# Optimization experiments

Hardware: AMD Instinct MI355X
Metric: run time of the kernel (lower is better)

Reference implementation:

```python
import jax, jax.numpy as jnp
import numpy as np

_SAMPLING_EPS = 1e-5


def setup_inputs() -> dict:
    key = jax.random.key(0)
    ks = jax.random.split(key, 7)
    N, V, H = 256, 128000, 200  # num_seqs, vocab_size, output-history length
    logits = jax.random.normal(ks[0], (N, V), dtype=jnp.float32)
    output_tokens = jax.random.randint(ks[1], (N, H), 0, V, dtype=jnp.int32)
    presence_penalties = jax.random.uniform(ks[2], (N,), jnp.float32, 0.0, 2.0)
    frequency_penalties = jax.random.uniform(ks[3], (N,), jnp.float32, 0.0, 2.0)
    temperatures = jax.random.uniform(ks[4], (N,), jnp.float32, 0.5, 1.5)
    top_ps = jax.random.uniform(ks[5], (N,), jnp.float32, 0.5, 1.0)
    top_ks = jax.random.randint(ks[6], (N,), 1, 1000, dtype=jnp.int32)
    return {
        "logits": logits,
        "presence_penalties": presence_penalties,
        "frequency_penalties": frequency_penalties,
        "temperatures": temperatures,
        "top_ps": top_ps,
        "output_tokens": output_tokens,
        "top_ks": top_ks,
    }


def reference(logits, presence_penalties, frequency_penalties, temperatures,
              top_ps, output_tokens, top_ks):
    N, V = logits.shape

    # ---- _apply_penalties: bincount of previously generated tokens per row ----
    rows = jnp.arange(N)[:, None]  # [N,1] broadcast against [N,H] token ids
    bin_counts = jnp.zeros((N, V), logits.dtype).at[rows, output_tokens].add(1.0)
    # rows are skipped when both penalties are < eps (original builds an index list)
    active = ((presence_penalties >= _SAMPLING_EPS) |
              (frequency_penalties >= _SAMPLING_EPS))[:, None]
    presence_mask = (bin_counts > 0.0).astype(logits.dtype)
    penalty = (frequency_penalties[:, None] * bin_counts
               + presence_penalties[:, None] * presence_mask)
    logits = logits - jnp.where(active, penalty, jnp.zeros((), logits.dtype))

    # ---- temperature scaling + softmax ----
    logits = logits / temperatures[:, None]
    probs = jax.nn.softmax(logits, axis=-1)

    # ---- _apply_top_p_top_k: sort desc, cumsum, mask, unsort ----
    probs_idx = jnp.argsort(-probs, axis=-1)                    # descending order
    probs_sort = jnp.take_along_axis(probs, probs_idx, axis=-1)
    probs_sum = jnp.cumsum(probs_sort, axis=-1)
    top_p_mask = (probs_sum - probs_sort) > top_ps[:, None]     # exclusive cumsum > p
    probs_sort = jnp.where(top_p_mask, 0.0, probs_sort)
    top_k_mask = jnp.arange(V, dtype=top_ks.dtype)[None, :] >= top_ks[:, None]
    probs_sort = jnp.where(top_k_mask, 0.0, probs_sort)
    inv_idx = jnp.argsort(probs_idx, axis=-1)                   # unsort permutation
    filtered_probs = jnp.take_along_axis(probs_sort, inv_idx, axis=-1)
    return filtered_probs
```

## Files before the change

kernel.cpp:

```cpp
#include <hip/hip_runtime.h>
#include <stdint.h>

#define NB 4096
#define BSH 20
#define RSH 14
#define HS 512
#define HM 511
#define CAP 8192
#define PCAP 4096
#define NRB 2048
#define NT 1024

typedef unsigned long long ull;

__device__ __forceinline__ unsigned mono_u32(float x) {
    unsigned b = __float_as_uint(x);
    return (b & 0x80000000u) ? ~b : (b | 0x80000000u);
}
__device__ __forceinline__ float inv_mono(unsigned u) {
    unsigned b = (u & 0x80000000u) ? (u & 0x7fffffffu) : ~u;
    return __uint_as_float(b);
}

__device__ __forceinline__ float compute_x(float l, int cnt,
                                           float pres, float freq, float t) {
    float pen = __fadd_rn(__fmul_rn(freq, (float)cnt), (cnt > 0) ? pres : 0.0f);
    return __fdiv_rn(__fsub_rn(l, pen), t);
}

__device__ __forceinline__ int hash_lookup(const int* hkey, const int* hval, int v) {
    unsigned h = ((unsigned)v * 2654435761u) >> 23;
    while (true) {
        int kk = hkey[h];
        if (kk == v) return hval[h];
        if (kk == -1) return 0;
        h = (h + 1) & HM;
    }
}

__device__ int suffix_cut(unsigned* hc, int* sct, int* sct2, int k, int tid, int* sh) {
    if (tid == 0) *sh = -1;
    const int BPT = NB / NT;
    int base = tid * BPT;
    int acc = 0;
#pragma unroll
    for (int q = BPT - 1; q >= 0; --q) { acc += (int)hc[base + q]; hc[base + q] = (unsigned)acc; }
    sct[tid] = acc;
    __syncthreads();
    int* a = sct; int* b2 = sct2;
    for (int s = 1; s < NT; s <<= 1) {
        int v = a[tid] + ((tid + s < NT) ? a[tid + s] : 0);
        __syncthreads();
        b2[tid] = v;
        __syncthreads();
        int* tmp = a; a = b2; b2 = tmp;
    }
    int above = (tid < NT - 1) ? a[tid + 1] : 0;
    int best = -1;
#pragma unroll
    for (int q = BPT - 1; q >= 0; --q)
        if ((int)hc[base + q] + above >= k) { best = base + q; break; }
    if (best >= 0) atomicMax(sh, best);
    __syncthreads();
    int r = *sh;
    __syncthreads();
    return r;
}

__global__ __launch_bounds__(NT) void k_fused(
    const float* __restrict__ logits, const int* __restrict__ tokens,
    const float* __restrict__ pres_v, const float* __restrict__ freq_v,
    const float* __restrict__ temps, const float* __restrict__ topp_v,
    const int* __restrict__ topk_v, int V, int H, float* __restrict__ out)
{
    __shared__ ull skey[CAP];
    __shared__ ull hreg[4096];
    __shared__ int sct[NT], sct2[NT];
    __shared__ int hkey[HS], hval[HS];
    __shared__ float esum_s, corr_s;
    __shared__ int cut_s, lcnt_s, rb_s, pcnt_s;

    unsigned* hc = (unsigned*)hreg;
    unsigned* rh = (unsigned*)hreg;
    ull* tmpc = hreg;
    float* se = (float*)hreg;
    float* bs1 = (float*)sct;
    float* bs2 = (float*)sct2;

    int row = blockIdx.x, tid = threadIdx.x;
    for (int b = tid; b < NB; b += NT) hc[b] = 0u;
    for (int i = tid; i < HS; i += NT) { hkey[i] = -1; hval[i] = 0; }
    if (tid == 0) { esum_s = 0.f; corr_s = 0.f; lcnt_s = 0; rb_s = 0; pcnt_s = 0; }
    __syncthreads();

    const int* trow = tokens + (size_t)row * H;
    for (int i = tid; i < H; i += NT) {
        int v = trow[i];
        unsigned h = ((unsigned)v * 2654435761u) >> 23;
        while (true) {
            int prev = atomicCAS(&hkey[h], -1, v);
            if (prev == -1 || prev == v) { atomicAdd(&hval[h], 1); break; }
            h = (h + 1) & HM;
        }
    }

    float t = temps[row];
    float r = __fdiv_rn(1.0f, t);
    float pres = pres_v[row], freq = freq_v[row];
    int active = (pres >= 1e-5f) || (freq >= 1e-5f);
    int k = topk_v[row];
    const float* lrow = logits + (size_t)row * V;
    const float4* l4p = (const float4*)lrow;
    int V4 = V >> 2;
    __syncthreads();

    int S4 = V4 >> 4;
    for (int j = tid; j < S4; j += NT) {
        int c = j >> 6;
        int g = (((c << 4) + (c & 15)) << 6) | (j & 63);
        if (g < V4) {
            float4 A = l4p[g];
#pragma unroll
            for (int jj = 0; jj < 4; ++jj)
                atomicAdd(&hc[mono_u32(__fmul_rn((&A.x)[jj], r)) >> BSH], 1u);
        }
    }
    __syncthreads();
    float ms = (S4 > 0) ? ((float)k * (float)(S4 << 2) / (float)V) : 0.0f;
    int req = (int)(ms + 8.0f * sqrtf(ms) + 16.0f);
    int bT = (S4 > 0) ? suffix_cut(hc, sct, sct2, req, tid, &cut_s) : 0;
    int thr = bT - 1; if (thr < 0) thr = 0;
    for (int b = tid; b < NB; b += NT) hc[b] = 0u;
    __syncthreads();

    float4* o4p = (float4*)(out + (size_t)row * V);
    const float4 z4 = make_float4(0.f, 0.f, 0.f, 0.f);
    float es0 = 0.f, es1 = 0.f, es2 = 0.f, es3 = 0.f;
    int i = tid;
    for (; i + 7 * NT < V4; i += 8 * NT) {
        float4 arr[8];
#pragma unroll
        for (int q = 0; q < 8; ++q) arr[q] = l4p[i + q * NT];
#pragma unroll
        for (int q = 0; q < 8; ++q) o4p[i + q * NT] = z4;
#pragma unroll
        for (int q = 0; q < 8; ++q) {
            int vb = (i + q * NT) << 2;
            float x0 = __fmul_rn(arr[q].x, r), x1 = __fmul_rn(arr[q].y, r);
            float x2 = __fmul_rn(arr[q].z, r), x3 = __fmul_rn(arr[q].w, r);
            es0 += __expf(x0); es1 += __expf(x1); es2 += __expf(x2); es3 += __expf(x3);
            unsigned u0 = mono_u32(x0), u1 = mono_u32(x1);
            unsigned u2 = mono_u32(x2), u3 = mono_u32(x3);
            if ((int)(u0 >> BSH) >= thr) {
                atomicAdd(&hc[u0 >> BSH], 1u);
                int pos = atomicAdd(&lcnt_s, 1);
                if (pos < CAP) skey[pos] = ((ull)u0 << 32) | (unsigned)~(unsigned)(vb);
            }
            if ((int)(u1 >> BSH) >= thr) {
                atomicAdd(&hc[u1 >> BSH], 1u);
                int pos = atomicAdd(&lcnt_s, 1);
                if (pos < CAP) skey[pos] = ((ull)u1 << 32) | (unsigned)~(unsigned)(vb + 1);
            }
            if ((int)(u2 >> BSH) >= thr) {
                atomicAdd(&hc[u2 >> BSH], 1u);
                int pos = atomicAdd(&lcnt_s, 1);
                if (pos < CAP) skey[pos] = ((ull)u2 << 32) | (unsigned)~(unsigned)(vb + 2);
            }
            if ((int)(u3 >> BSH) >= thr) {
                atomicAdd(&hc[u3 >> BSH], 1u);
                int pos = atomicAdd(&lcnt_s, 1);
                if (pos < CAP) skey[pos] = ((ull)u3 << 32) | (unsigned)~(unsigned)(vb + 3);
            }
        }
    }
    for (; i < V4; i += NT) {
        float4 A = l4p[i];
        o4p[i] = z4;
#pragma unroll
        for (int j = 0; j < 4; ++j) {
            float x = __fmul_rn((&A.x)[j], r);
            es0 += __expf(x);
            unsigned u = mono_u32(x);
            if ((int)(u >> BSH) >= thr) {
                atomicAdd(&hc[u >> BSH], 1u);
                int pos = atomicAdd(&lcnt_s, 1);
                if (pos < CAP) skey[pos] = ((ull)u << 32) | (unsigned)~(unsigned)((i << 2) + j);
            }
        }
    }
    for (int v = (V4 << 2) + tid; v < V; v += NT) {
        float x = __fmul_rn(lrow[v], r);
        out[(size_t)row * V + v] = 0.0f;
        es0 += __expf(x);
        unsigned u = mono_u32(x);
        if ((int)(u >> BSH) >= thr) {
            atomicAdd(&hc[u >> BSH], 1u);
            int pos = atomicAdd(&lcnt_s, 1);
            if (pos < CAP) skey[pos] = ((ull)u << 32) | (unsigned)~(unsigned)v;
        }
    }
    float es = (es0 + es1) + (es2 + es3);
    for (int off = 32; off; off >>= 1) es += __shfl_down(es, off);
    if ((tid & 63) == 0) atomicAdd(&esum_s, es);
    __syncthreads();

    float corr = 0.0f;
    if (active) {
        for (int s = tid; s < HS; s += NT) {
            int v = hkey[s];
            if (v >= 0) {
                int c = hval[s];
                float l = lrow[v];
                float x0 = __fmul_rn(l, r);
                float xp = compute_x(l, c, pres, freq, t);
                int b0 = (int)(mono_u32(x0) >> BSH);
                int bp = (int)(mono_u32(xp) >> BSH);
                if (b0 != bp) {
                    if (b0 >= thr) atomicSub(&hc[b0], 1u);
                    if (bp >= thr) atomicAdd(&hc[bp], 1u);
                }
                corr += __expf(xp) - __expf(x0);
            }
        }
    }
    for (int off = 32; off; off >>= 1) corr += __shfl_down(corr, off);
    if ((tid & 63) == 0) atomicAdd(&corr_s, corr);
    __syncthreads();
    int lraw = lcnt_s;
    int count = lraw > CAP ? CAP : lraw;

    for (int j = tid; j < count; j += NT) {
        unsigned idx = ~(unsigned)(skey[j] & 0xffffffffull);
        float l = lrow[idx];
        int c = active ? hash_lookup(hkey, hval, (int)idx) : 0;
        unsigned ue = (c > 0) ? mono_u32(compute_x(l, c, pres, freq, t))
                              : mono_u32(__fdiv_rn(l, t));
        skey[j] = ((ull)ue << 32) | (unsigned)~idx;
    }
    __syncthreads();

    int bst = suffix_cut(hc, sct, sct2, k, tid, &cut_s);
    bool ok = (bst >= thr + 2) && (lraw <= CAP);

    if (!ok) {
        for (int b = tid; b < NB; b += NT) hc[b] = 0u;
        if (tid == 0) lcnt_s = 0;
        __syncthreads();
        for (int v = tid; v < V; v += NT)
            atomicAdd(&hc[mono_u32(__fmul_rn(lrow[v], r)) >> BSH], 1u);
        __syncthreads();
        if (active) {
            for (int s = tid; s < HS; s += NT) {
                int v = hkey[s];
                if (v >= 0) {
                    int c = hval[s];
                    float l = lrow[v];
                    int b0 = (int)(mono_u32(__fmul_rn(l, r)) >> BSH);
                    int bp = (int)(mono_u32(compute_x(l, c, pres, freq, t)) >> BSH);
                    if (b0 != bp) { atomicSub(&hc[b0], 1u); atomicAdd(&hc[bp], 1u); }
                }
            }
        }
        __syncthreads();
        bst = suffix_cut(hc, sct, sct2, k, tid, &cut_s);
        int thr2 = bst - 2; if (thr2 < 0) thr2 = 0;
        for (int v = tid; v < V; v += NT) {
            unsigned u = mono_u32(__fmul_rn(lrow[v], r));
            if ((int)(u >> BSH) >= thr2) {
                int pos = atomicAdd(&lcnt_s, 1);
                if (pos < CAP) skey[pos] = ((ull)u << 32) | (unsigned)~(unsigned)v;
            }
        }
        __syncthreads();
        count = lcnt_s > CAP ? CAP : lcnt_s;
        for (int j = tid; j < count; j += NT) {
            unsigned idx = ~(unsigned)(skey[j] & 0xffffffffull);
            float l = lrow[idx];
            int c = active ? hash_lookup(hkey, hval, (int)idx) : 0;
            unsigned ue = (c > 0) ? mono_u32(compute_x(l, c, pres, freq, t))
                                  : mono_u32(__fdiv_rn(l, t));
            skey[j] = ((ull)ue << 32) | (unsigned)~idx;
        }
        __syncthreads();
    }
    float Sp = esum_s + corr_s;

    for (int g = tid; g < NRB; g += NT) rh[g] = 0u;
    __syncthreads();
    int gmin = (bst - 1) << 6;
    for (int j = tid; j < count; j += NT) {
        unsigned u = (unsigned)(skey[j] >> 32);
        int rel = (int)(u >> RSH) - gmin;
        rel = rel < 0 ? 0 : (rel > NRB - 1 ? NRB - 1 : rel);
        atomicAdd(&rh[rel], 1u);
    }
    __syncthreads();
    {
        int b2i = tid * 2;
        int a2 = (int)rh[b2i + 1];
        rh[b2i + 1] = (unsigned)a2;
        a2 += (int)rh[b2i];
        rh[b2i] = (unsigned)a2;
        sct[tid] = a2;
        __syncthreads();
        int* a = sct; int* b2 = sct2;
        for (int s = 1; s < NT; s <<= 1) {
            int v = a[tid] + ((tid + s < NT) ? a[tid + s] : 0);
            __syncthreads();
            b2[tid] = v;
            __syncthreads();
            int* tmp = a; a = b2; b2 = tmp;
        }
        int above = (tid < NT - 1) ? a[tid + 1] : 0;
        int best = -1;
        if ((int)rh[b2i + 1] + above >= k) best = b2i + 1;
        else if ((int)rh[b2i] + above >= k) best = b2i;
        if (best >= 0) atomicMax(&rb_s, best);
    }
    __syncthreads();
    int rb = rb_s;
    for (int j = tid; j < count; j += NT) {
        unsigned u = (unsigned)(skey[j] >> 32);
        int rel = (int)(u >> RSH) - gmin;
        rel = rel < 0 ? 0 : (rel > NRB - 1 ? NRB - 1 : rel);
        if (rel >= rb) {
            int pos = atomicAdd(&pcnt_s, 1);
            if (pos < PCAP) tmpc[pos] = skey[j];
        }
    }
    __syncthreads();
    int count2 = pcnt_s;
    if (count2 <= PCAP) {
        for (int j = tid; j < count2; j += NT) skey[j] = tmpc[j];
        count = count2;
    }
    __syncthreads();

    int m = 1; while (m < count) m <<= 1;
    for (int j = count + tid; j < m; j += NT) skey[j] = 0ull;
    __syncthreads();
    for (int kk = 2; kk <= m; kk <<= 1) {
        for (int jj = kk >> 1; jj > 0; jj >>= 1) {
            for (int i2 = tid; i2 < m; i2 += NT) {
                int ixj = i2 ^ jj;
                if (ixj > i2) {
                    ull A = skey[i2], B = skey[ixj];
                    bool up = ((i2 & kk) != 0);
                    if ((A > B) == up) { skey[i2] = B; skey[ixj] = A; }
                }
            }
            __syncthreads();
        }
    }

    for (int j = tid; j < CAP; j += NT)
        se[j] = (j < count) ? __expf(inv_mono((unsigned)(skey[j] >> 32))) : 0.0f;
    __syncthreads();
    int j0 = tid << 3;
    float ee[8], cc[8];
    float run = 0.0f;
#pragma unroll
    for (int q = 0; q < 8; ++q) { ee[q] = se[j0 + q]; run += ee[q]; cc[q] = run; }
    bs1[tid] = run;
    __syncthreads();
    float* a = bs1; float* b2 = bs2;
    for (int s = 1; s < NT; s <<= 1) {
        float v = a[tid] + ((tid >= s) ? a[tid - s] : 0.0f);
        __syncthreads();
        b2[tid] = v;
        __syncthreads();
        float* tmp = a; a = b2; b2 = tmp;
    }
    float pre = (tid > 0) ? a[tid - 1] : 0.0f;

    float pS = topp_v[row] * Sp;
#pragma unroll
    for (int q = 0; q < 8; ++q) {
        int j = j0 + q;
        if (j < count) {
            float e = ee[q];
            float excl = __fsub_rn(pre + cc[q], e);
            if ((j < k) && (excl <= pS)) {
                unsigned idx = ~(unsigned)(skey[j] & 0xffffffffull);
                out[(size_t)row * V + idx] = __fdiv_rn(e, Sp);
            }
        }
    }
}

extern "C" void kernel_launch(void* const* d_in, const int* in_sizes, int n_in,
                              void* d_out, int out_size, void* d_ws, size_t ws_size,
                              hipStream_t stream) {
    const float* logits = (const float*)d_in[0];
    const float* pres   = (const float*)d_in[1];
    const float* freq   = (const float*)d_in[2];
    const float* temps  = (const float*)d_in[3];
    const float* topps  = (const float*)d_in[4];
    const int*   tokens = (const int*)d_in[5];
    const int*   topks  = (const int*)d_in[6];
    int N = in_sizes[1];
    int V = in_sizes[0] / N;
    int H = in_sizes[5] / N;
    float* out = (float*)d_out;

    k_fused<<<N, NT, 0, stream>>>(logits, tokens, pres, freq, temps, topps,
                                  topks, V, H, out);
}
```

Baseline: 303.7 us.

## Warp-specialize zero-fill and scan, use wave-shuffle scans, skip refine for small counts

Splits the block so 256 threads zero-fill the output with nontemporal stores while 768 threads stream logits with nontemporal loads for the exp-sum, histogram and candidate collection. The shared-memory Hillis-Steele block scans are replaced by wave-shuffle scans with a 16-entry cross-wave combine, which removes many barriers. The second radix refinement pass now runs only when more than 2048 candidates were collected. The cost is fewer threads on the compute path and a possible load imbalance between the two thread groups.

```diff
diff --git a/kernel.cpp b/kernel.cpp
--- a/kernel.cpp
+++ b/kernel.cpp
@@ -10,8 +10,12 @@
 #define PCAP 4096
 #define NRB 2048
 #define NT 1024
+#define NW 16
+#define NTS 256
+#define NTC 768
 
 typedef unsigned long long ull;
+typedef float vf4 __attribute__((ext_vector_type(4)));
 
 __device__ __forceinline__ unsigned mono_u32(float x) {
     unsigned b = __float_as_uint(x);
@@ -38,28 +42,32 @@
     }
 }
 
-__device__ int suffix_cut(unsigned* hc, int* sct, int* sct2, int k, int tid, int* sh) {
+__device__ __forceinline__ int wave_suffix_above(int acc, int tid, int* wq) {
+    int lane = tid & 63, wv = tid >> 6;
+    int v = acc;
+#pragma unroll
+    for (int off = 1; off < 64; off <<= 1) {
+        int x = __shfl_down(v, off);
+        if (lane + off < 64) v += x;
+    }
+    if (lane == 0) wq[wv] = v;
+    __syncthreads();
+    int ws = 0;
+    for (int w = wv + 1; w < NW; ++w) ws += wq[w];
+    return (v - acc) + ws;
+}
+
+__device__ int suffix_cut4(const unsigned* hc, int* wq, int* sh, int k, int tid) {
     if (tid == 0) *sh = -1;
-    const int BPT = NB / NT;
-    int base = tid * BPT;
-    int acc = 0;
-#pragma unroll
-    for (int q = BPT - 1; q >= 0; --q) { acc += (int)hc[base + q]; hc[base + q] = (unsigned)acc; }
-    sct[tid] = acc;
-    __syncthreads();
-    int* a = sct; int* b2 = sct2;
-    for (int s = 1; s < NT; s <<= 1) {
-        int v = a[tid] + ((tid + s < NT) ? a[tid + s] : 0);
-        __syncthreads();
-        b2[tid] = v;
-        __syncthreads();
-        int* tmp = a; a = b2; b2 = tmp;
-    }
-    int above = (tid < NT - 1) ? a[tid + 1] : 0;
+    int base = tid * 4;
+    int c0 = hc[base], c1 = hc[base + 1], c2 = hc[base + 2], c3 = hc[base + 3];
+    int s3 = c3, s2 = s3 + c2, s1 = s2 + c1, s0 = s1 + c0;
+    int above = wave_suffix_above(s0, tid, wq);
     int best = -1;
-#pragma unroll
-    for (int q = BPT - 1; q >= 0; --q)
-        if ((int)hc[base + q] + above >= k) { best = base + q; break; }
+    if (s3 + above >= k) best = base + 3;
+    else if (s2 + above >= k) best = base + 2;
+    else if (s1 + above >= k) best = base + 1;
+    else if (s0 + above >= k) best = base + 0;
     if (best >= 0) atomicMax(sh, best);
     __syncthreads();
     int r = *sh;
@@ -75,17 +83,14 @@
 {
     __shared__ ull skey[CAP];
     __shared__ ull hreg[4096];
-    __shared__ int sct[NT], sct2[NT];
     __shared__ int hkey[HS], hval[HS];
+    __shared__ int wqi[NW];
+    __shared__ float wqf[NW];
     __shared__ float esum_s, corr_s;
     __shared__ int cut_s, lcnt_s, rb_s, pcnt_s;
 
     unsigned* hc = (unsigned*)hreg;
-    unsigned* rh = (unsigned*)hreg;
-    ull* tmpc = hreg;
     float* se = (float*)hreg;
-    float* bs1 = (float*)sct;
-    float* bs2 = (float*)sct2;
 
     int row = blockIdx.x, tid = threadIdx.x;
     for (int b = tid; b < NB; b += NT) hc[b] = 0u;
@@ -110,98 +115,109 @@
     int active = (pres >= 1e-5f) || (freq >= 1e-5f);
     int k = topk_v[row];
     const float* lrow = logits + (size_t)row * V;
-    const float4* l4p = (const float4*)lrow;
+    const vf4* l4p = (const vf4*)lrow;
     int V4 = V >> 2;
     __syncthreads();
 
     int S4 = V4 >> 4;
-    for (int j = tid; j < S4; j += NT) {
-        int c = j >> 6;
-        int g = (((c << 4) + (c & 15)) << 6) | (j & 63);
-        if (g < V4) {
-            float4 A = l4p[g];
-#pragma unroll
-            for (int jj = 0; jj < 4; ++jj)
-                atomicAdd(&hc[mono_u32(__fmul_rn((&A.x)[jj], r)) >> BSH], 1u);
+    if (tid >= NTS) {
+        for (int j = tid - NTS; j < S4; j += NTC) {
+            int c = j >> 6;
+            int g = (((c << 4) + (c & 15)) << 6) | (j & 63);
+            if (g < V4) {
+                vf4 A = l4p[g];
+#pragma unroll
+                for (int jj = 0; jj < 4; ++jj)
+                    atomicAdd(&hc[mono_u32(__fmul_rn(A[jj], r)) >> BSH], 1u);
+            }
         }
     }
     __syncthreads();
     float ms = (S4 > 0) ? ((float)k * (float)(S4 << 2) / (float)V) : 0.0f;
     int req = (int)(ms + 8.0f * sqrtf(ms) + 16.0f);
-    int bT = (S4 > 0) ? suffix_cut(hc, sct, sct2, req, tid, &cut_s) : 0;
+    int bT = (S4 > 0) ? suffix_cut4(hc, wqi, &cut_s, req, tid) : 0;
     int thr = bT - 1; if (thr < 0) thr = 0;
     for (int b = tid; b < NB; b += NT) hc[b] = 0u;
     __syncthreads();
 
-    float4* o4p = (float4*)(out + (size_t)row * V);
-    const float4 z4 = make_float4(0.f, 0.f, 0.f, 0.f);
-    float es0 = 0.f, es1 = 0.f, es2 = 0.f, es3 = 0.f;
-    int i = tid;
-    for (; i + 7 * NT < V4; i += 8 * NT) {
-        float4 arr[8];
-#pragma unroll
-        for (int q = 0; q < 8; ++q) arr[q] = l4p[i + q * NT];
-#pragma unroll
-        for (int q = 0; q < 8; ++q) o4p[i + q * NT] = z4;
-#pragma unroll
-        for (int q = 0; q < 8; ++q) {
-            int vb = (i + q * NT) << 2;
-            float x0 = __fmul_rn(arr[q].x, r), x1 = __fmul_rn(arr[q].y, r);
-            float x2 = __fmul_rn(arr[q].z, r), x3 = __fmul_rn(arr[q].w, r);
-            es0 += __expf(x0); es1 += __expf(x1); es2 += __expf(x2); es3 += __expf(x3);
-            unsigned u0 = mono_u32(x0), u1 = mono_u32(x1);
-            unsigned u2 = mono_u32(x2), u3 = mono_u32(x3);
-            if ((int)(u0 >> BSH) >= thr) {
-                atomicAdd(&hc[u0 >> BSH], 1u);
-                int pos = atomicAdd(&lcnt_s, 1);
-                if (pos < CAP) skey[pos] = ((ull)u0 << 32) | (unsigned)~(unsigned)(vb);
-            }
-            if ((int)(u1 >> BSH) >= thr) {
-                atomicAdd(&hc[u1 >> BSH], 1u);
-                int pos = atomicAdd(&lcnt_s, 1);
-                if (pos < CAP) skey[pos] = ((ull)u1 << 32) | (unsigned)~(unsigned)(vb + 1);
-            }
-            if ((int)(u2 >> BSH) >= thr) {
-                atomicAdd(&hc[u2 >> BSH], 1u);
-                int pos = atomicAdd(&lcnt_s, 1);
-                if (pos < CAP) skey[pos] = ((ull)u2 << 32) | (unsigned)~(unsigned)(vb + 2);
-            }
-            if ((int)(u3 >> BSH) >= thr) {
-                atomicAdd(&hc[u3 >> BSH], 1u);
-                int pos = atomicAdd(&lcnt_s, 1);
-                if (pos < CAP) skey[pos] = ((ull)u3 << 32) | (unsigned)~(unsigned)(vb + 3);
-            }
-        }
-    }
-    for (; i < V4; i += NT) {
-        float4 A = l4p[i];
-        o4p[i] = z4;
-#pragma unroll
-        for (int j = 0; j < 4; ++j) {
-            float x = __fmul_rn((&A.x)[j], r);
+    vf4* o4p = (vf4*)(out + (size_t)row * V);
+    if (tid < NTS) {
+        vf4 z4 = {0.f, 0.f, 0.f, 0.f};
+        int i = tid;
+        for (; i + 7 * NTS < V4; i += 8 * NTS) {
+#pragma unroll
+            for (int q = 0; q < 8; ++q)
+                __builtin_nontemporal_store(z4, &o4p[i + q * NTS]);
+        }
+        for (; i < V4; i += NTS) __builtin_nontemporal_store(z4, &o4p[i]);
+        for (int v = (V4 << 2) + tid; v < V; v += NTS) out[(size_t)row * V + v] = 0.0f;
+    } else {
+        int ctid = tid - NTS;
+        float es0 = 0.f, es1 = 0.f, es2 = 0.f, es3 = 0.f;
+        int i = ctid;
+        for (; i + 7 * NTC < V4; i += 8 * NTC) {
+            vf4 arr[8];
+#pragma unroll
+            for (int q = 0; q < 8; ++q)
+                arr[q] = __builtin_nontemporal_load(&l4p[i + q * NTC]);
+#pragma unroll
+            for (int q = 0; q < 8; ++q) {
+                int vb = (i + q * NTC) << 2;
+                float x0 = __fmul_rn(arr[q][0], r), x1 = __fmul_rn(arr[q][1], r);
+                float x2 = __fmul_rn(arr[q][2], r), x3 = __fmul_rn(arr[q][3], r);
+                es0 += __expf(x0); es1 += __expf(x1); es2 += __expf(x2); es3 += __expf(x3);
+                unsigned u0 = mono_u32(x0), u1 = mono_u32(x1);
+                unsigned u2 = mono_u32(x2), u3 = mono_u32(x3);
+                if ((int)(u0 >> BSH) >= thr) {
+                    atomicAdd(&hc[u0 >> BSH], 1u);
+                    int pos = atomicAdd(&lcnt_s, 1);
+                    if (pos < CAP) skey[pos] = ((ull)u0 << 32) | (unsigned)~(unsigned)(vb);
+                }
+                if ((int)(u1 >> BSH) >= thr) {
+                    atomicAdd(&hc[u1 >> BSH], 1u);
+                    int pos = atomicAdd(&lcnt_s, 1);
+                    if (pos < CAP) skey[pos] = ((ull)u1 << 32) | (unsigned)~(unsigned)(vb + 1);
+                }
+                if ((int)(u2 >> BSH) >= thr) {
+                    atomicAdd(&hc[u2 >> BSH], 1u);
+                    int pos = atomicAdd(&lcnt_s, 1);
+                    if (pos < CAP) skey[pos] = ((ull)u2 << 32) | (unsigned)~(unsigned)(vb + 2);
+                }
+                if ((int)(u3 >> BSH) >= thr) {
+                    atomicAdd(&hc[u3 >> BSH], 1u);
+                    int pos = atomicAdd(&lcnt_s, 1);
+                    if (pos < CAP) skey[pos] = ((ull)u3 << 32) | (unsigned)~(unsigned)(vb + 3);
+                }
+            }
+        }
+        for (; i < V4; i += NTC) {
+            vf4 A = __builtin_nontemporal_load(&l4p[i]);
+#pragma unroll
+            for (int j = 0; j < 4; ++j) {
+                float x = __fmul_rn(A[j], r);
+                es0 += __expf(x);
+                unsigned u = mono_u32(x);
+                if ((int)(u >> BSH) >= thr) {
+                    atomicAdd(&hc[u >> BSH], 1u);
+                    int pos = atomicAdd(&lcnt_s, 1);
+                    if (pos < CAP) skey[pos] = ((ull)u << 32) | (unsigned)~(unsigned)((i << 2) + j);
+                }
+            }
+        }
+        for (int v = (V4 << 2) + ctid; v < V; v += NTC) {
+            float x = __fmul_rn(lrow[v], r);
             es0 += __expf(x);
             unsigned u = mono_u32(x);
             if ((int)(u >> BSH) >= thr) {
                 atomicAdd(&hc[u >> BSH], 1u);
                 int pos = atomicAdd(&lcnt_s, 1);
-                if (pos < CAP) skey[pos] = ((ull)u << 32) | (unsigned)~(unsigned)((i << 2) + j);
-            }
-        }
-    }
-    for (int v = (V4 << 2) + tid; v < V; v += NT) {
-        float x = __fmul_rn(lrow[v], r);
-        out[(size_t)row * V + v] = 0.0f;
-        es0 += __expf(x);
-        unsigned u = mono_u32(x);
-        if ((int)(u >> BSH) >= thr) {
-            atomicAdd(&hc[u >> BSH], 1u);
-            int pos = atomicAdd(&lcnt_s, 1);
-            if (pos < CAP) skey[pos] = ((ull)u << 32) | (unsigned)~(unsigned)v;
-        }
-    }
-    float es = (es0 + es1) + (es2 + es3);
-    for (int off = 32; off; off >>= 1) es += __shfl_down(es, off);
-    if ((tid & 63) == 0) atomicAdd(&esum_s, es);
+                if (pos < CAP) skey[pos] = ((ull)u << 32) | (unsigned)~(unsigned)v;
+            }
+        }
+        float es = (es0 + es1) + (es2 + es3);
+        for (int off = 32; off; off >>= 1) es += __shfl_down(es, off);
+        if ((tid & 63) == 0) atomicAdd(&esum_s, es);
+    }
     __syncthreads();
 
     float corr = 0.0f;
@@ -239,7 +255,7 @@
     }
     __syncthreads();
 
-    int bst = suffix_cut(hc, sct, sct2, k, tid, &cut_s);
+    int bst = suffix_cut4(hc, wqi, &cut_s, k, tid);
     bool ok = (bst >= thr + 2) && (lraw <= CAP);
 
     if (!ok) {
@@ -262,7 +278,7 @@
             }
         }
         __syncthreads();
-        bst = suffix_cut(hc, sct, sct2, k, tid, &cut_s);
+        bst = suffix_cut4(hc, wqi, &cut_s, k, tid);
         int thr2 = bst - 2; if (thr2 < 0) thr2 = 0;
         for (int v = tid; v < V; v += NT) {
             unsigned u = mono_u32(__fmul_rn(lrow[v], r));
@@ -285,56 +301,46 @@
     }
     float Sp = esum_s + corr_s;
 
-    for (int g = tid; g < NRB; g += NT) rh[g] = 0u;
-    __syncthreads();
-    int gmin = (bst - 1) << 6;
-    for (int j = tid; j < count; j += NT) {
-        unsigned u = (unsigned)(skey[j] >> 32);
-        int rel = (int)(u >> RSH) - gmin;
-        rel = rel < 0 ? 0 : (rel > NRB - 1 ? NRB - 1 : rel);
-        atomicAdd(&rh[rel], 1u);
-    }
-    __syncthreads();
-    {
+    if (count > 2048) {
+        unsigned* rh = (unsigned*)hreg;
+        for (int g = tid; g < NRB; g += NT) rh[g] = 0u;
+        __syncthreads();
+        int gmin = (bst - 1) << 6;
+        for (int j = tid; j < count; j += NT) {
+            unsigned u = (unsigned)(skey[j] >> 32);
+            int rel = (int)(u >> RSH) - gmin;
+            rel = rel < 0 ? 0 : (rel > NRB - 1 ? NRB - 1 : rel);
+            atomicAdd(&rh[rel], 1u);
+        }
+        __syncthreads();
         int b2i = tid * 2;
-        int a2 = (int)rh[b2i + 1];
-        rh[b2i + 1] = (unsigned)a2;
-        a2 += (int)rh[b2i];
-        rh[b2i] = (unsigned)a2;
-        sct[tid] = a2;
-        __syncthreads();
-        int* a = sct; int* b2 = sct2;
-        for (int s = 1; s < NT; s <<= 1) {
-            int v = a[tid] + ((tid + s < NT) ? a[tid + s] : 0);
-            __syncthreads();
-            b2[tid] = v;
-            __syncthreads();
-            int* tmp = a; a = b2; b2 = tmp;
-        }
-        int above = (tid < NT - 1) ? a[tid + 1] : 0;
+        int d0 = rh[b2i], d1 = rh[b2i + 1];
+        int t1 = d1, t0 = d1 + d0;
+        int above = wave_suffix_above(t0, tid, wqi);
         int best = -1;
-        if ((int)rh[b2i + 1] + above >= k) best = b2i + 1;
-        else if ((int)rh[b2i] + above >= k) best = b2i;
+        if (t1 + above >= k) best = b2i + 1;
+        else if (t0 + above >= k) best = b2i;
         if (best >= 0) atomicMax(&rb_s, best);
-    }
-    __syncthreads();
-    int rb = rb_s;
-    for (int j = tid; j < count; j += NT) {
-        unsigned u = (unsigned)(skey[j] >> 32);
-        int rel = (int)(u >> RSH) - gmin;
-        rel = rel < 0 ? 0 : (rel > NRB - 1 ? NRB - 1 : rel);
-        if (rel >= rb) {
-            int pos = atomicAdd(&pcnt_s, 1);
-            if (pos < PCAP) tmpc[pos] = skey[j];
-        }
-    }
-    __syncthreads();
-    int count2 = pcnt_s;
-    if (count2 <= PCAP) {
-        for (int j = tid; j < count2; j += NT) skey[j] = tmpc[j];
-        count = count2;
-    }
-    __syncthreads();
+        __syncthreads();
+        int rb = rb_s;
+        ull* tmpc = hreg;
+        for (int j = tid; j < count; j += NT) {
+            unsigned u = (unsigned)(skey[j] >> 32);
+            int rel = (int)(u >> RSH) - gmin;
+            rel = rel < 0 ? 0 : (rel > NRB - 1 ? NRB - 1 : rel);
+            if (rel >= rb) {
+                int pos = atomicAdd(&pcnt_s, 1);
+                if (pos < PCAP) tmpc[pos] = skey[j];
+            }
+        }
+        __syncthreads();
+        int count2 = pcnt_s;
+        if (count2 <= PCAP) {
+            for (int j = tid; j < count2; j += NT) skey[j] = tmpc[j];
+            count = count2;
+        }
+        __syncthreads();
+    }
 
     int m = 1; while (m < count) m <<= 1;
     for (int j = count + tid; j < m; j += NT) skey[j] = 0ull;
@@ -361,28 +367,31 @@
     float run = 0.0f;
 #pragma unroll
     for (int q = 0; q < 8; ++q) { ee[q] = se[j0 + q]; run += ee[q]; cc[q] = run; }
-    bs1[tid] = run;
-    __syncthreads();
-    float* a = bs1; float* b2 = bs2;
-    for (int s = 1; s < NT; s <<= 1) {
-        float v = a[tid] + ((tid >= s) ? a[tid - s] : 0.0f);
-        __syncthreads();
-        b2[tid] = v;
-        __syncthreads();
-        float* tmp = a; a = b2; b2 = tmp;
-    }
-    float pre = (tid > 0) ? a[tid - 1] : 0.0f;
-
-    float pS = topp_v[row] * Sp;
-#pragma unroll
-    for (int q = 0; q < 8; ++q) {
-        int j = j0 + q;
-        if (j < count) {
-            float e = ee[q];
-            float excl = __fsub_rn(pre + cc[q], e);
-            if ((j < k) && (excl <= pS)) {
-                unsigned idx = ~(unsigned)(skey[j] & 0xffffffffull);
-                out[(size_t)row * V + idx] = __fdiv_rn(e, Sp);
+    {
+        int lane = tid & 63, wv = tid >> 6;
+        float v = run;
+#pragma unroll
+        for (int off = 1; off < 64; off <<= 1) {
+            float x = __shfl_up(v, off);
+            if (lane >= off) v += x;
+        }
+        if (lane == 63) wqf[wv] = v;
+        __syncthreads();
+        float wpre = 0.0f;
+        for (int w = 0; w < wv; ++w) wpre += wqf[w];
+        float pre = wpre + (v - run);
+
+        float pS = topp_v[row] * Sp;
+#pragma unroll
+        for (int q = 0; q < 8; ++q) {
+            int j = j0 + q;
+            if (j < count) {
+                float e = ee[q];
+                float excl = __fsub_rn(pre + cc[q], e);
+                if ((j < k) && (excl <= pS)) {
+                    unsigned idx = ~(unsigned)(skey[j] & 0xffffffffull);
+                    out[(size_t)row * V + idx] = __fdiv_rn(e, Sp);
+                }
             }
         }
     }
```

Result: no change. 309.2 us (+1.8%).
